# Kernel optimization log

Measured on AMD Instinct MI355X. Metric: run time of the kernel, lower is better.

The kernel has to match this reference:

```python
import jax, jax.numpy as jnp
import numpy as np

B, F, D, E = 16384, 2048, 256, 8  # batch, feature, expert out dim, n instrument experts (+1 default)


def setup_inputs() -> dict:
    key = jax.random.key(0)
    k1, k2, k3 = jax.random.split(key, 3)
    shared_features = jax.random.normal(k1, (B, F), dtype=jnp.float32)
    # instrument ids 0..E-1; id_to_index is the identity mapping here
    instrument_ids = jax.random.randint(k2, (B, 1), 0, E, dtype=jnp.int32)
    # stacked expert weights: E instrument layers + 1 default layer => E+1 Dense(F->D)
    W = jax.random.normal(k3, (E + 1, F, D), dtype=jnp.float32) * 0.02
    b = jnp.zeros((E + 1, D), dtype=jnp.float32)
    return {"shared_features": shared_features, "W": W, "b": b,
            "instrument_ids": instrument_ids}


def reference(shared_features, W, b, instrument_ids):
    # Compute ALL expert projections on the full batch (faithful to the TF layer),
    # stacked on axis=1: [B, E+1, D]
    stacked = jnp.einsum('bf,efd->bed', shared_features, W) + b
    # id_to_index lookup: ids are 0..E-1, identity mapping; default layer at index E unused
    idx = instrument_ids[:, 0].astype(jnp.int32)  # [B]
    # gather_nd equivalent: select per-sample expert output -> [B, D]
    selected = jnp.take_along_axis(stacked, idx[:, None, None], axis=1)[:, 0, :]
    return selected
```

## Files before the change

kernel.cpp:

```cpp
#include <hip/hip_runtime.h>
#include <hip/hip_bf16.h>

#define B_SZ 16384
#define F_SZ 2048
#define D_SZ 256
#define E_SZ 8
#define GRID_G 184
#define XCHUNK (GRID_G / 8)

typedef __attribute__((ext_vector_type(8))) short bhalf8;
typedef __attribute__((ext_vector_type(4))) float fl4;

__device__ __forceinline__ short f2b(float f) {
  __hip_bfloat16 h = __float2bfloat16(f);
  union { __hip_bfloat16 h; short s; } u;
  u.h = h;
  return u.s;
}

__global__ void k_scatter(const int* __restrict__ ids, int* __restrict__ counts,
                          int* __restrict__ perm) {
  __shared__ int lcnt[E_SZ], lbase[E_SZ];
  int t = threadIdx.x;
  if (t < E_SZ) lcnt[t] = 0;
  __syncthreads();
  int b = blockIdx.x * 256 + t;
  int e = ids[b];
  int p = atomicAdd(&lcnt[e], 1);
  __syncthreads();
  if (t < E_SZ) lbase[t] = atomicAdd(&counts[t], lcnt[t]);
  __syncthreads();
  perm[e * B_SZ + lbase[e] + p] = b;
}

__global__ void k_transpose(const float* __restrict__ W, __hip_bfloat16* __restrict__ Wt) {
  __shared__ float tile[64][65];
  int e = blockIdx.z;
  int f0 = blockIdx.x * 64;
  int d0 = blockIdx.y * 64;
  int t = threadIdx.x;
  const float* src = W + ((size_t)e * F_SZ + f0) * D_SZ + d0;
  int fr = t >> 2, c0 = t & 3;
#pragma unroll
  for (int c = c0; c < 16; c += 4) {
    float4 v = *(const float4*)(src + (size_t)fr * D_SZ + c * 4);
    tile[fr][c * 4 + 0] = v.x;
    tile[fr][c * 4 + 1] = v.y;
    tile[fr][c * 4 + 2] = v.z;
    tile[fr][c * 4 + 3] = v.w;
  }
  __syncthreads();
  int dr = t >> 2, cc = t & 3;
  union { unsigned short u[16]; bhalf8 v[2]; } pk;
#pragma unroll
  for (int k = 0; k < 16; ++k) pk.u[k] = (unsigned short)f2b(tile[cc * 16 + k][dr]);
  __hip_bfloat16* dst = Wt + ((size_t)e * D_SZ + d0 + dr) * F_SZ + f0 + cc * 16;
  ((bhalf8*)dst)[0] = pk.v[0];
  ((bhalf8*)dst)[1] = pk.v[1];
}

__device__ __forceinline__ void load_lds16(const __hip_bfloat16* g, __hip_bfloat16* l) {
  __builtin_amdgcn_global_load_lds((const __attribute__((address_space(1))) void*)g,
                                   (__attribute__((address_space(3))) void*)l, 16, 0, 0);
}

__launch_bounds__(512, 2)
__global__ void k_gemm(const float* __restrict__ x, const __hip_bfloat16* __restrict__ Wt,
                       const float* __restrict__ bias, const int* __restrict__ counts,
                       const int* __restrict__ perm, float* __restrict__ out) {
  int bid = blockIdx.x;
  int mt = (bid & 7) * XCHUNK + (bid >> 3);
  int e = -1, mbase = 0, count = 0;
  {
    int acc0 = 0;
#pragma unroll
    for (int ee = 0; ee < E_SZ; ++ee) {
      int c = counts[ee];
      int nt = (c + 95) / 96;
      if (e < 0 && mt < acc0 + nt) { e = ee; mbase = (mt - acc0) * 96; count = c; }
      acc0 += nt;
    }
  }
  if (e < 0) return;

  __shared__ __align__(16) __hip_bfloat16 As[2 * 96 * 64];
  __shared__ __align__(16) __hip_bfloat16 Bs[3 * 256 * 64];

  int t = threadIdx.x;
  int w = t >> 6;
  int lane = t & 63;
  int wm = w >> 2, wn = w & 3;
  int l15 = lane & 15;
  int q = lane >> 4;

  const int* permE = perm + e * B_SZ;

  int tr = t >> 4;
  int tc = t & 15;
  const float* pA[3];
  int wAo[3];
#pragma unroll
  for (int i = 0; i < 3; ++i) {
    int r = i * 32 + tr;
    int gm = mbase + r;
    int src = permE[(gm < count) ? gm : mbase];
    pA[i] = x + (size_t)src * F_SZ + tc * 4;
    int cw = tc >> 1, half = tc & 1;
    wAo[i] = r * 64 + ((cw ^ (r & 7)) * 8) + half * 4;
  }

  const __hip_bfloat16* pB[4];
  int dB[4];
#pragma unroll
  for (int i = 0; i < 4; ++i) {
    int p = i * 512 + t;
    int n = p >> 3;
    int cl = (p & 7) ^ (n & 7);
    pB[i] = Wt + (size_t)(e * D_SZ + n) * F_SZ + cl * 8;
    dB[i] = i * 4096 + w * 512;
  }

  int rAo[2][3], rBo[2][4];
#pragma unroll
  for (int ks = 0; ks < 2; ++ks) {
#pragma unroll
    for (int i = 0; i < 3; ++i) {
      int m = wm * 48 + i * 16 + l15;
      rAo[ks][i] = m * 64 + (((ks * 4 + q) ^ (m & 7)) * 8);
    }
#pragma unroll
    for (int j = 0; j < 4; ++j) {
      int n = wn * 64 + j * 16 + l15;
      rBo[ks][j] = n * 64 + (((ks * 4 + q) ^ (n & 7)) * 8);
    }
  }

  fl4 zz = {0.0f, 0.0f, 0.0f, 0.0f};
  fl4 acc[3][4];
#pragma unroll
  for (int i = 0; i < 3; ++i)
#pragma unroll
    for (int j = 0; j < 4; ++j) acc[i][j] = zz;

  float4 avA[3], avB[3];

#pragma unroll
  for (int i = 0; i < 4; ++i) load_lds16(pB[i], Bs + dB[i]);
#pragma unroll
  for (int i = 0; i < 4; ++i) load_lds16(pB[i] + 64, Bs + 16384 + dB[i]);
  __builtin_amdgcn_sched_barrier(0);
  {
    float4 avP[3];
#pragma unroll
    for (int i = 0; i < 3; ++i) avP[i] = *(const float4*)(pA[i]);
#pragma unroll
    for (int i = 0; i < 3; ++i) {
      short4 s;
      s.x = f2b(avP[i].x); s.y = f2b(avP[i].y);
      s.z = f2b(avP[i].z); s.w = f2b(avP[i].w);
      *(short4*)(As + wAo[i]) = s;
    }
  }
#pragma unroll
  for (int i = 0; i < 3; ++i) avA[i] = *(const float4*)(pA[i] + 64);
#pragma unroll
  for (int i = 0; i < 3; ++i) avB[i] = *(const float4*)(pA[i] + 128);
  __builtin_amdgcn_sched_barrier(0);
  asm volatile("s_waitcnt vmcnt(6) lgkmcnt(0)");
  __builtin_amdgcn_sched_barrier(0);
  __builtin_amdgcn_s_barrier();
  __builtin_amdgcn_sched_barrier(0);

#define ITER(kk, AV, MB, DB, MA, DA)                                                  \
  do {                                                                                \
    _Pragma("unroll")                                                                 \
    for (int i = 0; i < 4; ++i)                                                       \
      load_lds16(pB[i] + ((kk) + 2) * 64, Bs + (DB) * 16384 + dB[i]);                 \
    __builtin_amdgcn_sched_barrier(0);                                                \
    _Pragma("unroll")                                                                 \
    for (int i = 0; i < 3; ++i) {                                                     \
      short4 s;                                                                       \
      s.x = f2b(AV[i].x); s.y = f2b(AV[i].y);                                         \
      s.z = f2b(AV[i].z); s.w = f2b(AV[i].w);                                         \
      *(short4*)(As + (DA) * 6144 + wAo[i]) = s;                                      \
    }                                                                                 \
    {                                                                                 \
      int kn_ = ((kk) + 3) & 31;                                                      \
      _Pragma("unroll")                                                               \
      for (int i = 0; i < 3; ++i) AV[i] = *(const float4*)(pA[i] + kn_ * 64);         \
    }                                                                                 \
    {                                                                                 \
      const __hip_bfloat16* Ab_ = As + (MA) * 6144;                                   \
      const __hip_bfloat16* Bb_ = Bs + (MB) * 16384;                                  \
      _Pragma("unroll")                                                               \
      for (int ks = 0; ks < 2; ++ks) {                                                \
        bhalf8 af[3], bf[4];                                                          \
        _Pragma("unroll")                                                             \
        for (int i = 0; i < 3; ++i) af[i] = *(const bhalf8*)(Ab_ + rAo[ks][i]);       \
        _Pragma("unroll")                                                             \
        for (int j = 0; j < 4; ++j) bf[j] = *(const bhalf8*)(Bb_ + rBo[ks][j]);       \
        _Pragma("unroll")                                                             \
        for (int i = 0; i < 3; ++i)                                                   \
          _Pragma("unroll")                                                           \
          for (int j = 0; j < 4; ++j)                                                 \
            acc[i][j] = __builtin_amdgcn_mfma_f32_16x16x32_bf16(af[i], bf[j],         \
                                                                acc[i][j], 0, 0, 0); \
      }                                                                               \
    }                                                                                 \
    __builtin_amdgcn_sched_barrier(0);                                                \
    asm volatile("s_waitcnt vmcnt(10) lgkmcnt(0)");                                   \
    __builtin_amdgcn_sched_barrier(0);                                                \
    __builtin_amdgcn_s_barrier();                                                     \
    __builtin_amdgcn_sched_barrier(0);                                                \
  } while (0)

  for (int k = 0; k < 30; k += 6) {
    ITER(k + 0, avA, 0, 2, 0, 1);
    ITER(k + 1, avB, 1, 0, 1, 0);
    ITER(k + 2, avA, 2, 1, 0, 1);
    ITER(k + 3, avB, 0, 2, 1, 0);
    ITER(k + 4, avA, 1, 0, 0, 1);
    ITER(k + 5, avB, 2, 1, 1, 0);
  }
#undef ITER

  {
#pragma unroll
    for (int i = 0; i < 3; ++i) {
      short4 s;
      s.x = f2b(avA[i].x); s.y = f2b(avA[i].y);
      s.z = f2b(avA[i].z); s.w = f2b(avA[i].w);
      *(short4*)(As + 6144 + wAo[i]) = s;
    }
    const __hip_bfloat16* Ab = As;
    const __hip_bfloat16* Bb = Bs;
#pragma unroll
    for (int ks = 0; ks < 2; ++ks) {
      bhalf8 af[3], bf[4];
#pragma unroll
      for (int i = 0; i < 3; ++i) af[i] = *(const bhalf8*)(Ab + rAo[ks][i]);
#pragma unroll
      for (int j = 0; j < 4; ++j) bf[j] = *(const bhalf8*)(Bb + rBo[ks][j]);
#pragma unroll
      for (int i = 0; i < 3; ++i)
#pragma unroll
        for (int j = 0; j < 4; ++j)
          acc[i][j] = __builtin_amdgcn_mfma_f32_16x16x32_bf16(af[i], bf[j], acc[i][j], 0, 0, 0);
    }
  }
  __builtin_amdgcn_sched_barrier(0);
  asm volatile("s_waitcnt vmcnt(3) lgkmcnt(0)");
  __builtin_amdgcn_sched_barrier(0);
  __builtin_amdgcn_s_barrier();
  __builtin_amdgcn_sched_barrier(0);
  asm volatile("" :: "v"(avB[0].x), "v"(avB[1].x), "v"(avB[2].x));

  {
    const __hip_bfloat16* Ab = As + 6144;
    const __hip_bfloat16* Bb = Bs + 16384;
#pragma unroll
    for (int ks = 0; ks < 2; ++ks) {
      bhalf8 af[3], bf[4];
#pragma unroll
      for (int i = 0; i < 3; ++i) af[i] = *(const bhalf8*)(Ab + rAo[ks][i]);
#pragma unroll
      for (int j = 0; j < 4; ++j) bf[j] = *(const bhalf8*)(Bb + rBo[ks][j]);
#pragma unroll
      for (int i = 0; i < 3; ++i)
#pragma unroll
        for (int j = 0; j < 4; ++j)
          acc[i][j] = __builtin_amdgcn_mfma_f32_16x16x32_bf16(af[i], bf[j], acc[i][j], 0, 0, 0);
    }
  }

  float bv[4];
#pragma unroll
  for (int j = 0; j < 4; ++j) bv[j] = bias[e * D_SZ + wn * 64 + j * 16 + l15];

#pragma unroll
  for (int i = 0; i < 3; ++i) {
#pragma unroll
    for (int r = 0; r < 4; ++r) {
      int gm = mbase + wm * 48 + i * 16 + q * 4 + r;
      if (gm < count) {
        int row = permE[gm];
        float* po = out + (size_t)row * D_SZ + wn * 64;
#pragma unroll
        for (int j = 0; j < 4; ++j) po[j * 16 + l15] = acc[i][j][r] + bv[j];
      }
    }
  }
}

extern "C" void kernel_launch(void* const* d_in, const int* in_sizes, int n_in,
                              void* d_out, int out_size, void* d_ws, size_t ws_size,
                              hipStream_t stream) {
  const float* x = (const float*)d_in[0];
  const float* W = (const float*)d_in[1];
  const float* bias = (const float*)d_in[2];
  const int* ids = (const int*)d_in[3];
  float* out = (float*)d_out;

  char* ws = (char*)d_ws;
  int* counts = (int*)ws;
  int* perm = (int*)(ws + 256);
  __hip_bfloat16* Wt = (__hip_bfloat16*)(ws + (1 << 20));

  hipMemsetAsync(counts, 0, E_SZ * sizeof(int), stream);
  k_scatter<<<B_SZ / 256, 256, 0, stream>>>(ids, counts, perm);
  k_transpose<<<dim3(F_SZ / 64, D_SZ / 64, E_SZ), 256, 0, stream>>>(W, Wt);
  k_gemm<<<GRID_G, 512, 0, stream>>>(x, Wt, bias, counts, perm, out);
}
```

Measured before the change: 236.9 us.

## Split K in half with larger M tiles and add a reduction kernel

The grouped GEMM now uses 160-row M tiles and splits the K dimension into two halves, so each block handles one half of the 2048 features. Partial sums go to a workspace buffer, and a new reduce kernel adds them, applies the bias and scatters rows back through the permutation. The aim is more blocks per tile of weights, better load balance across CUs and better reuse of the B tile per A row. The cost is extra global traffic for the partials, an extra kernel launch, and more registers for the 5x4 accumulator set.

```diff
diff --git a/kernel.cpp b/kernel.cpp
--- a/kernel.cpp
+++ b/kernel.cpp
@@ -5,8 +5,9 @@
 #define F_SZ 2048
 #define D_SZ 256
 #define E_SZ 8
-#define GRID_G 184
+#define GRID_G 224
 #define XCHUNK (GRID_G / 8)
+#define TMAX 112
 
 typedef __attribute__((ext_vector_type(8))) short bhalf8;
 typedef __attribute__((ext_vector_type(4))) float fl4;
@@ -66,24 +67,26 @@
 
 __launch_bounds__(512, 2)
 __global__ void k_gemm(const float* __restrict__ x, const __hip_bfloat16* __restrict__ Wt,
-                       const float* __restrict__ bias, const int* __restrict__ counts,
-                       const int* __restrict__ perm, float* __restrict__ out) {
+                       const int* __restrict__ counts, const int* __restrict__ perm,
+                       float* __restrict__ part) {
   int bid = blockIdx.x;
-  int mt = (bid & 7) * XCHUNK + (bid >> 3);
+  int id = (bid & 7) * XCHUNK + (bid >> 3);
+  int tile = id >> 1;
+  int khalf = id & 1;
   int e = -1, mbase = 0, count = 0;
   {
     int acc0 = 0;
 #pragma unroll
     for (int ee = 0; ee < E_SZ; ++ee) {
       int c = counts[ee];
-      int nt = (c + 95) / 96;
-      if (e < 0 && mt < acc0 + nt) { e = ee; mbase = (mt - acc0) * 96; count = c; }
+      int nt = (c + 159) / 160;
+      if (e < 0 && tile < acc0 + nt) { e = ee; mbase = (tile - acc0) * 160; count = c; }
       acc0 += nt;
     }
   }
   if (e < 0) return;
 
-  __shared__ __align__(16) __hip_bfloat16 As[2 * 96 * 64];
+  __shared__ __align__(16) __hip_bfloat16 As[2 * 160 * 64];
   __shared__ __align__(16) __hip_bfloat16 Bs[3 * 256 * 64];
 
   int t = threadIdx.x;
@@ -94,17 +97,18 @@
   int q = lane >> 4;
 
   const int* permE = perm + e * B_SZ;
+  const int kbase = khalf * 1024;
 
   int tr = t >> 4;
   int tc = t & 15;
-  const float* pA[3];
-  int wAo[3];
-#pragma unroll
-  for (int i = 0; i < 3; ++i) {
+  const float* pA[5];
+  int wAo[5];
+#pragma unroll
+  for (int i = 0; i < 5; ++i) {
     int r = i * 32 + tr;
     int gm = mbase + r;
     int src = permE[(gm < count) ? gm : mbase];
-    pA[i] = x + (size_t)src * F_SZ + tc * 4;
+    pA[i] = x + (size_t)src * F_SZ + kbase + tc * 4;
     int cw = tc >> 1, half = tc & 1;
     wAo[i] = r * 64 + ((cw ^ (r & 7)) * 8) + half * 4;
   }
@@ -116,16 +120,16 @@
     int p = i * 512 + t;
     int n = p >> 3;
     int cl = (p & 7) ^ (n & 7);
-    pB[i] = Wt + (size_t)(e * D_SZ + n) * F_SZ + cl * 8;
+    pB[i] = Wt + (size_t)(e * D_SZ + n) * F_SZ + kbase + cl * 8;
     dB[i] = i * 4096 + w * 512;
   }
 
-  int rAo[2][3], rBo[2][4];
+  int rAo[2][5], rBo[2][4];
 #pragma unroll
   for (int ks = 0; ks < 2; ++ks) {
 #pragma unroll
-    for (int i = 0; i < 3; ++i) {
-      int m = wm * 48 + i * 16 + l15;
+    for (int i = 0; i < 5; ++i) {
+      int m = wm * 80 + i * 16 + l15;
       rAo[ks][i] = m * 64 + (((ks * 4 + q) ^ (m & 7)) * 8);
     }
 #pragma unroll
@@ -136,13 +140,13 @@
   }
 
   fl4 zz = {0.0f, 0.0f, 0.0f, 0.0f};
-  fl4 acc[3][4];
-#pragma unroll
-  for (int i = 0; i < 3; ++i)
+  fl4 acc[5][4];
+#pragma unroll
+  for (int i = 0; i < 5; ++i)
 #pragma unroll
     for (int j = 0; j < 4; ++j) acc[i][j] = zz;
 
-  float4 avA[3], avB[3];
+  float4 avA[5], avB[5];
 
 #pragma unroll
   for (int i = 0; i < 4; ++i) load_lds16(pB[i], Bs + dB[i]);
@@ -150,11 +154,11 @@
   for (int i = 0; i < 4; ++i) load_lds16(pB[i] + 64, Bs + 16384 + dB[i]);
   __builtin_amdgcn_sched_barrier(0);
   {
-    float4 avP[3];
-#pragma unroll
-    for (int i = 0; i < 3; ++i) avP[i] = *(const float4*)(pA[i]);
-#pragma unroll
-    for (int i = 0; i < 3; ++i) {
+    float4 avP[5];
+#pragma unroll
+    for (int i = 0; i < 5; ++i) avP[i] = *(const float4*)(pA[i]);
+#pragma unroll
+    for (int i = 0; i < 5; ++i) {
       short4 s;
       s.x = f2b(avP[i].x); s.y = f2b(avP[i].y);
       s.z = f2b(avP[i].z); s.w = f2b(avP[i].w);
@@ -162,11 +166,11 @@
     }
   }
 #pragma unroll
-  for (int i = 0; i < 3; ++i) avA[i] = *(const float4*)(pA[i] + 64);
-#pragma unroll
-  for (int i = 0; i < 3; ++i) avB[i] = *(const float4*)(pA[i] + 128);
-  __builtin_amdgcn_sched_barrier(0);
-  asm volatile("s_waitcnt vmcnt(6) lgkmcnt(0)");
+  for (int i = 0; i < 5; ++i) avA[i] = *(const float4*)(pA[i] + 64);
+#pragma unroll
+  for (int i = 0; i < 5; ++i) avB[i] = *(const float4*)(pA[i] + 128);
+  __builtin_amdgcn_sched_barrier(0);
+  asm volatile("s_waitcnt vmcnt(10) lgkmcnt(0)");
   __builtin_amdgcn_sched_barrier(0);
   __builtin_amdgcn_s_barrier();
   __builtin_amdgcn_sched_barrier(0);
@@ -178,29 +182,29 @@
       load_lds16(pB[i] + ((kk) + 2) * 64, Bs + (DB) * 16384 + dB[i]);                 \
     __builtin_amdgcn_sched_barrier(0);                                                \
     _Pragma("unroll")                                                                 \
-    for (int i = 0; i < 3; ++i) {                                                     \
+    for (int i = 0; i < 5; ++i) {                                                     \
       short4 s;                                                                       \
       s.x = f2b(AV[i].x); s.y = f2b(AV[i].y);                                         \
       s.z = f2b(AV[i].z); s.w = f2b(AV[i].w);                                         \
-      *(short4*)(As + (DA) * 6144 + wAo[i]) = s;                                      \
+      *(short4*)(As + (DA) * 10240 + wAo[i]) = s;                                     \
     }                                                                                 \
     {                                                                                 \
-      int kn_ = ((kk) + 3) & 31;                                                      \
+      int kn_ = ((kk) + 3) & 15;                                                      \
       _Pragma("unroll")                                                               \
-      for (int i = 0; i < 3; ++i) AV[i] = *(const float4*)(pA[i] + kn_ * 64);         \
+      for (int i = 0; i < 5; ++i) AV[i] = *(const float4*)(pA[i] + kn_ * 64);         \
     }                                                                                 \
     {                                                                                 \
-      const __hip_bfloat16* Ab_ = As + (MA) * 6144;                                   \
+      const __hip_bfloat16* Ab_ = As + (MA) * 10240;                                  \
       const __hip_bfloat16* Bb_ = Bs + (MB) * 16384;                                  \
       _Pragma("unroll")                                                               \
       for (int ks = 0; ks < 2; ++ks) {                                                \
-        bhalf8 af[3], bf[4];                                                          \
+        bhalf8 af[5], bf[4];                                                          \
         _Pragma("unroll")                                                             \
-        for (int i = 0; i < 3; ++i) af[i] = *(const bhalf8*)(Ab_ + rAo[ks][i]);       \
+        for (int i = 0; i < 5; ++i) af[i] = *(const bhalf8*)(Ab_ + rAo[ks][i]);       \
         _Pragma("unroll")                                                             \
         for (int j = 0; j < 4; ++j) bf[j] = *(const bhalf8*)(Bb_ + rBo[ks][j]);       \
         _Pragma("unroll")                                                             \
-        for (int i = 0; i < 3; ++i)                                                   \
+        for (int i = 0; i < 5; ++i)                                                   \
           _Pragma("unroll")                                                           \
           for (int j = 0; j < 4; ++j)                                                 \
             acc[i][j] = __builtin_amdgcn_mfma_f32_16x16x32_bf16(af[i], bf[j],         \
@@ -208,13 +212,13 @@
       }                                                                               \
     }                                                                                 \
     __builtin_amdgcn_sched_barrier(0);                                                \
-    asm volatile("s_waitcnt vmcnt(10) lgkmcnt(0)");                                   \
+    asm volatile("s_waitcnt vmcnt(14) lgkmcnt(0)");                                   \
     __builtin_amdgcn_sched_barrier(0);                                                \
     __builtin_amdgcn_s_barrier();                                                     \
     __builtin_amdgcn_sched_barrier(0);                                                \
   } while (0)
 
-  for (int k = 0; k < 30; k += 6) {
+  for (int k = 0; k < 12; k += 6) {
     ITER(k + 0, avA, 0, 2, 0, 1);
     ITER(k + 1, avB, 1, 0, 1, 0);
     ITER(k + 2, avA, 2, 1, 0, 1);
@@ -222,72 +226,110 @@
     ITER(k + 4, avA, 1, 0, 0, 1);
     ITER(k + 5, avB, 2, 1, 1, 0);
   }
+  ITER(12, avA, 0, 2, 0, 1);
+  ITER(13, avB, 1, 0, 1, 0);
 #undef ITER
 
   {
 #pragma unroll
-    for (int i = 0; i < 3; ++i) {
+    for (int i = 0; i < 5; ++i) {
       short4 s;
       s.x = f2b(avA[i].x); s.y = f2b(avA[i].y);
       s.z = f2b(avA[i].z); s.w = f2b(avA[i].w);
-      *(short4*)(As + 6144 + wAo[i]) = s;
+      *(short4*)(As + 10240 + wAo[i]) = s;
     }
     const __hip_bfloat16* Ab = As;
-    const __hip_bfloat16* Bb = Bs;
+    const __hip_bfloat16* Bb = Bs + 32768;
 #pragma unroll
     for (int ks = 0; ks < 2; ++ks) {
-      bhalf8 af[3], bf[4];
-#pragma unroll
-      for (int i = 0; i < 3; ++i) af[i] = *(const bhalf8*)(Ab + rAo[ks][i]);
+      bhalf8 af[5], bf[4];
+#pragma unroll
+      for (int i = 0; i < 5; ++i) af[i] = *(const bhalf8*)(Ab + rAo[ks][i]);
 #pragma unroll
       for (int j = 0; j < 4; ++j) bf[j] = *(const bhalf8*)(Bb + rBo[ks][j]);
 #pragma unroll
-      for (int i = 0; i < 3; ++i)
+      for (int i = 0; i < 5; ++i)
 #pragma unroll
         for (int j = 0; j < 4; ++j)
           acc[i][j] = __builtin_amdgcn_mfma_f32_16x16x32_bf16(af[i], bf[j], acc[i][j], 0, 0, 0);
     }
   }
   __builtin_amdgcn_sched_barrier(0);
-  asm volatile("s_waitcnt vmcnt(3) lgkmcnt(0)");
+  asm volatile("s_waitcnt vmcnt(5) lgkmcnt(0)");
   __builtin_amdgcn_sched_barrier(0);
   __builtin_amdgcn_s_barrier();
   __builtin_amdgcn_sched_barrier(0);
-  asm volatile("" :: "v"(avB[0].x), "v"(avB[1].x), "v"(avB[2].x));
-
-  {
-    const __hip_bfloat16* Ab = As + 6144;
-    const __hip_bfloat16* Bb = Bs + 16384;
+  asm volatile("" :: "v"(avB[0].x), "v"(avB[1].x), "v"(avB[2].x),
+                     "v"(avB[3].x), "v"(avB[4].x));
+
+  {
+    const __hip_bfloat16* Ab = As + 10240;
+    const __hip_bfloat16* Bb = Bs;
 #pragma unroll
     for (int ks = 0; ks < 2; ++ks) {
-      bhalf8 af[3], bf[4];
-#pragma unroll
-      for (int i = 0; i < 3; ++i) af[i] = *(const bhalf8*)(Ab + rAo[ks][i]);
+      bhalf8 af[5], bf[4];
+#pragma unroll
+      for (int i = 0; i < 5; ++i) af[i] = *(const bhalf8*)(Ab + rAo[ks][i]);
 #pragma unroll
       for (int j = 0; j < 4; ++j) bf[j] = *(const bhalf8*)(Bb + rBo[ks][j]);
 #pragma unroll
-      for (int i = 0; i < 3; ++i)
+      for (int i = 0; i < 5; ++i)
 #pragma unroll
         for (int j = 0; j < 4; ++j)
           acc[i][j] = __builtin_amdgcn_mfma_f32_16x16x32_bf16(af[i], bf[j], acc[i][j], 0, 0, 0);
     }
   }
 
-  float bv[4];
-#pragma unroll
-  for (int j = 0; j < 4; ++j) bv[j] = bias[e * D_SZ + wn * 64 + j * 16 + l15];
-
-#pragma unroll
-  for (int i = 0; i < 3; ++i) {
+  float* pp = part + (size_t)(tile * 2 + khalf) * 40960;
+#pragma unroll
+  for (int i = 0; i < 5; ++i) {
 #pragma unroll
     for (int r = 0; r < 4; ++r) {
-      int gm = mbase + wm * 48 + i * 16 + q * 4 + r;
-      if (gm < count) {
-        int row = permE[gm];
-        float* po = out + (size_t)row * D_SZ + wn * 64;
-#pragma unroll
-        for (int j = 0; j < 4; ++j) po[j * 16 + l15] = acc[i][j][r] + bv[j];
-      }
+      int m = wm * 80 + i * 16 + q * 4 + r;
+      float* po = pp + m * 256 + wn * 64;
+#pragma unroll
+      for (int j = 0; j < 4; ++j) po[j * 16 + l15] = acc[i][j][r];
+    }
+  }
+}
+
+__global__ void k_reduce(const float* __restrict__ part, const float* __restrict__ bias,
+                         const int* __restrict__ counts, const int* __restrict__ perm,
+                         float* __restrict__ out) {
+  int tile = blockIdx.x >> 3;
+  int sub = blockIdx.x & 7;
+  int e = -1, mbase = 0, count = 0;
+  {
+    int acc0 = 0;
+#pragma unroll
+    for (int ee = 0; ee < E_SZ; ++ee) {
+      int c = counts[ee];
+      int nt = (c + 159) / 160;
+      if (e < 0 && tile < acc0 + nt) { e = ee; mbase = (tile - acc0) * 160; count = c; }
+      acc0 += nt;
+    }
+  }
+  if (e < 0) return;
+  const int* permE = perm + e * B_SZ;
+  const float* p0 = part + (size_t)(tile * 2) * 40960;
+  const float* p1 = p0 + 40960;
+  int t = threadIdx.x;
+#pragma unroll
+  for (int v = 0; v < 5; ++v) {
+    int idx = v * 256 + t;
+    int m = sub * 20 + (idx >> 6);
+    int c4 = (idx & 63) * 4;
+    int gm = mbase + m;
+    if (gm < count) {
+      float4 a = *(const float4*)(p0 + m * 256 + c4);
+      float4 b = *(const float4*)(p1 + m * 256 + c4);
+      float4 bv = *(const float4*)(bias + e * D_SZ + c4);
+      float4 r;
+      r.x = a.x + b.x + bv.x;
+      r.y = a.y + b.y + bv.y;
+      r.z = a.z + b.z + bv.z;
+      r.w = a.w + b.w + bv.w;
+      *(float4*)(out + (size_t)permE[gm] * D_SZ + c4) = r;
     }
   }
 }
@@ -305,9 +347,11 @@
   int* counts = (int*)ws;
   int* perm = (int*)(ws + 256);
   __hip_bfloat16* Wt = (__hip_bfloat16*)(ws + (1 << 20));
+  float* part = (float*)(ws + (16 << 20));
 
   hipMemsetAsync(counts, 0, E_SZ * sizeof(int), stream);
   k_scatter<<<B_SZ / 256, 256, 0, stream>>>(ids, counts, perm);
   k_transpose<<<dim3(F_SZ / 64, D_SZ / 64, E_SZ), 256, 0, stream>>>(W, Wt);
-  k_gemm<<<GRID_G, 512, 0, stream>>>(x, Wt, bias, counts, perm, out);
-}
+  k_gemm<<<GRID_G, 512, 0, stream>>>(x, Wt, counts, perm, part);
+  k_reduce<<<TMAX * 8, 256, 0, stream>>>(part, bias, counts, perm, out);
+}
```

After: 247.2 us. +4.4%, slower.
